# Kernel tuning notes

Hardware: AMD Instinct MI355X
Metric: run time of the kernel (lower is better)

The kernel has to match this reference:

```python
import jax, jax.numpy as jnp
import numpy as np

B, S, D, O, E, R = 4, 2048, 4096, 4096, 8, 16
SCALING = 32.0 / 16.0      # lora_alpha / lora_rank
MAX_THRESHOLD = 0.125      # 1 / num_experts


def setup_inputs() -> dict:
    key = jax.random.key(0)
    ks = jax.random.split(key, 8)
    return {
        "x": jax.random.normal(ks[0], (B, S, D), jnp.float32),
        "W_base": jax.random.normal(ks[1], (O, D), jnp.float32) * (1.0 / np.sqrt(D)),
        "b_base": jax.random.normal(ks[2], (O,), jnp.float32) * 0.02,
        "W_gate": jax.random.normal(ks[3], (E, D), jnp.float32) * (1.0 / np.sqrt(D)),
        "W_thr": jax.random.normal(ks[4], (D,), jnp.float32) * (1.0 / np.sqrt(D)),
        "b_thr": jax.random.normal(ks[5], (1,), jnp.float32) * 0.02,
        "A_w": jax.random.normal(ks[6], (E, R, D), jnp.float32) * (1.0 / np.sqrt(D)),
        "B_w": jax.random.normal(ks[7], (E, O, R), jnp.float32) * (1.0 / np.sqrt(R)),
    }


def reference(x, W_base, b_base, W_gate, W_thr, b_thr, A_w, B_w):
    # base linear: [B,S,O]
    base = jnp.einsum("bsd,od->bso", x, W_base) + b_base

    xf = x.reshape(-1, D)                                   # [N,D]
    gate = jax.nn.softmax(xf @ W_gate.T, axis=-1)           # [N,E]
    thr = jax.nn.sigmoid(xf @ W_thr + b_thr[0]) * MAX_THRESHOLD  # [N]
    adapted = gate - thr[:, None]                           # [N,E]
    selected = (adapted >= 0).astype(x.dtype)               # [N,E]
    w = adapted * selected
    wsum = jnp.sum(w, axis=-1, keepdims=True)
    wsum = jnp.where(wsum == 0, jnp.ones_like(wsum), wsum)
    w = w / wsum                                            # [N,E]

    # LoRA experts, dense equivalent of gather/compute/scatter
    h = jnp.einsum("nd,erd->ner", xf, A_w)                  # [N,E,R]
    moe = jnp.einsum("ner,ne,eor->no", h, w, B_w) * SCALING  # [N,O]

    return base + moe.reshape(base.shape)
```

## Files before the change

kernel.cpp:

```cpp
#include <hip/hip_runtime.h>
#include <hip/hip_bf16.h>

typedef float  f32x4  __attribute__((ext_vector_type(4)));
typedef __bf16 bf16x8 __attribute__((ext_vector_type(8)));
typedef __bf16 bf16x4 __attribute__((ext_vector_type(4)));

#define N_TOK 8192
#define D_DIM 4096
#define O_DIM 4096
#define ER    128
#define KCAT  4224
#define BAUX_ROWS 160

__device__ __forceinline__ void gl_lds16(const void* g, void* l) {
  __builtin_amdgcn_global_load_lds(
      (const __attribute__((address_space(1))) void*)g,
      (__attribute__((address_space(3))) void*)l, 16, 0, 0);
}

__global__ __launch_bounds__(256) void convert_kernel(
    const float* __restrict__ x,  const float* __restrict__ Wb,
    const float* __restrict__ Bw, const float* __restrict__ Aw,
    const float* __restrict__ Wg, const float* __restrict__ Wthr,
    __bf16* __restrict__ xcat, __bf16* __restrict__ Wcat,
    __bf16* __restrict__ Baux)
{
  const int id = blockIdx.x * 256 + threadIdx.x;
  const float* src;
  __bf16* dst;
  if (id < 4194304) {
    int row = id >> 9, ch = id & 511;
    src = x + ((size_t)row << 12) + ch * 8;
    dst = xcat + (size_t)row * KCAT + ch * 8;
  } else if (id < 6291456) {
    int i2 = id - 4194304;
    int row = i2 >> 9, ch = i2 & 511;
    src = Wb + ((size_t)row << 12) + ch * 8;
    dst = Wcat + (size_t)row * KCAT + ch * 8;
  } else if (id < 6356992) {
    int i2 = id - 6291456;
    int o = i2 >> 4, ch = i2 & 15;
    int e = ch >> 1, r0 = (ch & 1) * 8;
    src = Bw + (((size_t)e << 12) + o) * 16 + r0;
    dst = Wcat + (size_t)o * KCAT + D_DIM + ch * 8;
  } else {
    int i2 = id - 6356992;
    int row = i2 >> 9, ch = i2 & 511;
    dst = Baux + ((size_t)row << 12) + ch * 8;
    if (row < 128)       src = Aw + ((size_t)row << 12) + ch * 8;
    else if (row < 136)  src = Wg + ((size_t)(row - 128) << 12) + ch * 8;
    else if (row == 136) src = Wthr + ch * 8;
    else {
      bf16x8 z = {};
      *(bf16x8*)dst = z;
      return;
    }
  }
  f32x4 a = *(const f32x4*)src;
  f32x4 b = *(const f32x4*)(src + 4);
  bf16x8 v = { (__bf16)a[0], (__bf16)a[1], (__bf16)a[2], (__bf16)a[3],
               (__bf16)b[0], (__bf16)b[1], (__bf16)b[2], (__bf16)b[3] };
  *(bf16x8*)dst = v;
}

__global__ __launch_bounds__(256) void gemm_aux(
    const __bf16* __restrict__ A,
    const __bf16* __restrict__ Bm,
    float* __restrict__ pbuf, int kchunk)
{
  __shared__ __bf16 As[128 * 64];
  __shared__ __bf16 Bs[BAUX_ROWS * 64];
  const int tid  = threadIdx.x;
  const int lane = tid & 63;
  const int wave = tid >> 6;
  const int wm = wave >> 1, wn = wave & 1;
  const int quad = lane >> 4, m16 = lane & 15;
  const int bm = blockIdx.x;
  const int kc = blockIdx.y;

  f32x4 acc[4][5] = {};

  for (int k0 = kc * kchunk; k0 < (kc + 1) * kchunk; k0 += 64) {
#pragma unroll
    for (int i = 0; i < 4; ++i) {
      int c = i * 256 + tid;
      int row = c >> 3;
      int gk = (c & 7) ^ (row & 7);
      gl_lds16(A + (size_t)(bm * 128 + row) * KCAT + k0 + gk * 8, As + c * 8);
    }
#pragma unroll
    for (int i = 0; i < 5; ++i) {
      int c = i * 256 + tid;
      int row = c >> 3;
      int gk = (c & 7) ^ (row & 7);
      gl_lds16(Bm + ((size_t)row << 12) + k0 + gk * 8, Bs + c * 8);
    }
    __syncthreads();
#pragma unroll
    for (int kk = 0; kk < 64; kk += 32) {
      bf16x8 af[4], bfr[5];
#pragma unroll
      for (int i = 0; i < 4; ++i) {
        int rr = wm * 64 + i * 16 + m16;
        int ck = (kk >> 3) + quad;
        af[i] = *(const bf16x8*)(As + rr * 64 + ((ck ^ (rr & 7)) * 8));
      }
#pragma unroll
      for (int j = 0; j < 5; ++j) {
        int rr = wn * 80 + j * 16 + m16;
        int ck = (kk >> 3) + quad;
        bfr[j] = *(const bf16x8*)(Bs + rr * 64 + ((ck ^ (rr & 7)) * 8));
      }
#pragma unroll
      for (int i = 0; i < 4; ++i)
#pragma unroll
        for (int j = 0; j < 5; ++j)
          acc[i][j] = __builtin_amdgcn_mfma_f32_16x16x32_bf16(af[i], bfr[j], acc[i][j], 0, 0, 0);
    }
    __syncthreads();
  }

#pragma unroll
  for (int j = 0; j < 5; ++j) {
    int col = wn * 80 + j * 16 + m16;
#pragma unroll
    for (int i = 0; i < 4; ++i) {
      int row0 = bm * 128 + wm * 64 + i * 16 + quad * 4;
#pragma unroll
      for (int r = 0; r < 4; ++r)
        pbuf[((size_t)kc * N_TOK + row0 + r) * BAUX_ROWS + col] = acc[i][j][r];
    }
  }
}

__global__ __launch_bounds__(256) void combine_kernel(
    const float* __restrict__ pbuf,
    const float* __restrict__ bthr,
    __bf16* __restrict__ xcat, int KC)
{
  const int tid = threadIdx.x;
  const int tok = tid >> 4, l16 = tid & 15;
  const int row = blockIdx.x * 16 + tok;

  __shared__ float logits[16][9];
  __shared__ float wts[16][8];

  float h[8];
  float lg = 0.f;
#pragma unroll
  for (int i = 0; i < 8; ++i) {
    int c = i * 16 + l16;
    float s = 0.f;
    for (int kc = 0; kc < KC; ++kc)
      s += pbuf[((size_t)kc * N_TOK + row) * BAUX_ROWS + c];
    h[i] = s;
  }
  {
    int c = 128 + l16;
    for (int kc = 0; kc < KC; ++kc)
      lg += pbuf[((size_t)kc * N_TOK + row) * BAUX_ROWS + c];
    if (l16 < 9) logits[tok][l16] = lg;
  }
  __syncthreads();
  if (l16 == 0) {
    float g[9];
#pragma unroll
    for (int e = 0; e < 9; ++e) g[e] = logits[tok][e];
    float m = g[0];
#pragma unroll
    for (int e = 1; e < 8; ++e) m = fmaxf(m, g[e]);
    float p[8], s = 0.f;
#pragma unroll
    for (int e = 0; e < 8; ++e) { p[e] = expf(g[e] - m); s += p[e]; }
    float thr = 0.125f / (1.f + expf(-(g[8] + bthr[0])));
    float ws = 0.f;
#pragma unroll
    for (int e = 0; e < 8; ++e) {
      float a = p[e] / s - thr;
      a = (a >= 0.f) ? a : 0.f;
      p[e] = a; ws += a;
    }
    if (ws == 0.f) ws = 1.f;
    float inv = 2.0f / ws;
#pragma unroll
    for (int e = 0; e < 8; ++e) wts[tok][e] = p[e] * inv;
  }
  __syncthreads();
#pragma unroll
  for (int i = 0; i < 8; ++i) {
    int c = i * 16 + l16;
    xcat[(size_t)row * KCAT + D_DIM + c] = (__bf16)(h[i] * wts[tok][c >> 4]);
  }
}

__global__ __launch_bounds__(256) void gemm_main(
    const __bf16* __restrict__ A,
    const __bf16* __restrict__ Bm,
    const float* __restrict__ bias,
    float* __restrict__ out)
{
  __shared__ __bf16 As[128 * 64];
  __shared__ __bf16 Bs[128 * 64];
  const int tid  = threadIdx.x;
  const int lane = tid & 63;
  const int wave = tid >> 6;
  const int wm = wave >> 1, wn = wave & 1;
  const int quad = lane >> 4, m16 = lane & 15;

  const int bid = blockIdx.x;
  const int group = bid >> 10;
  const int r_ = bid & 1023;
  const int bn = (group << 4) | (r_ & 15);
  const int bm = r_ >> 4;

  f32x4 acc[4][4] = {};

  for (int k0 = 0; k0 < KCAT; k0 += 64) {
#pragma unroll
    for (int i = 0; i < 4; ++i) {
      int c = i * 256 + tid;
      int row = c >> 3;
      int gk = (c & 7) ^ (row & 7);
      gl_lds16(A  + (size_t)(bm * 128 + row) * KCAT + k0 + gk * 8, As + c * 8);
      gl_lds16(Bm + (size_t)(bn * 128 + row) * KCAT + k0 + gk * 8, Bs + c * 8);
    }
    __syncthreads();
#pragma unroll
    for (int kk = 0; kk < 64; kk += 32) {
      bf16x8 af[4], bfr[4];
#pragma unroll
      for (int i = 0; i < 4; ++i) {
        int rr = wm * 64 + i * 16 + m16;
        int ck = (kk >> 3) + quad;
        af[i] = *(const bf16x8*)(As + rr * 64 + ((ck ^ (rr & 7)) * 8));
      }
#pragma unroll
      for (int j = 0; j < 4; ++j) {
        int rr = wn * 64 + j * 16 + m16;
        int ck = (kk >> 3) + quad;
        bfr[j] = *(const bf16x8*)(Bs + rr * 64 + ((ck ^ (rr & 7)) * 8));
      }
#pragma unroll
      for (int i = 0; i < 4; ++i)
#pragma unroll
        for (int j = 0; j < 4; ++j)
          acc[i][j] = __builtin_amdgcn_mfma_f32_16x16x32_bf16(af[i], bfr[j], acc[i][j], 0, 0, 0);
    }
    __syncthreads();
  }

#pragma unroll
  for (int j = 0; j < 4; ++j) {
    int col = bn * 128 + wn * 64 + j * 16 + m16;
    float bv = bias[col];
#pragma unroll
    for (int i = 0; i < 4; ++i) {
      int row0 = bm * 128 + wm * 64 + i * 16 + quad * 4;
#pragma unroll
      for (int r = 0; r < 4; ++r) {
        out[(size_t)(row0 + r) * O_DIM + col] = acc[i][j][r] + bv;
      }
    }
  }
}

extern "C" void kernel_launch(void* const* d_in, const int* in_sizes, int n_in,
                              void* d_out, int out_size, void* d_ws, size_t ws_size,
                              hipStream_t stream) {
  const float* x    = (const float*)d_in[0];
  const float* Wb   = (const float*)d_in[1];
  const float* bb   = (const float*)d_in[2];
  const float* Wg   = (const float*)d_in[3];
  const float* Wthr = (const float*)d_in[4];
  const float* bthr = (const float*)d_in[5];
  const float* Aw   = (const float*)d_in[6];
  const float* Bw   = (const float*)d_in[7];
  float* out = (float*)d_out;

  char* ws = (char*)d_ws;
  __bf16* xcat = (__bf16*)ws;
  __bf16* Wcat = (__bf16*)(ws + 69206016);
  __bf16* Baux = (__bf16*)(ws + 69206016 + 34603008);
  float*  pbuf = (float*)(ws + 105119744);

  int KC = 1;
  if (ws_size >= 105119744 + 4ull * 5242880) KC = 4;
  else if (ws_size >= 105119744 + 2ull * 5242880) KC = 2;

  convert_kernel<<<25152, 256, 0, stream>>>(x, Wb, Bw, Aw, Wg, Wthr, xcat, Wcat, Baux);
  dim3 agrid(64, KC);
  gemm_aux<<<agrid, 256, 0, stream>>>(xcat, Baux, pbuf, D_DIM / KC);
  combine_kernel<<<512, 256, 0, stream>>>(pbuf, bthr, xcat, KC);
  gemm_main<<<2048, 256, 0, stream>>>(xcat, Wcat, bb, out);
}
```

Before: 651.3 us.

## Rewrite main GEMM with 256x256 tiles and a 4-stage LDS pipeline

The main bf16 GEMM now uses 512-thread workgroups computing 256x256 output tiles, where it used 128x128. K-step loads go through a 4-slot ring of LDS buffers, prefetched two steps ahead with global_load_lds and waited on via explicit vmcnt and a single barrier per step. It also adds a rotating LDS swizzle, s_setprio around the MFMA block, and an XCD-aware block remap. The goal is more operand reuse per LDS load and overlap of memory traffic with MFMA work, at the cost of higher register pressure (128 accumulators per lane) and far fewer workgroups (512).

```diff
diff --git a/kernel.cpp b/kernel.cpp
--- a/kernel.cpp
+++ b/kernel.cpp
@@ -11,6 +11,7 @@
 #define ER    128
 #define KCAT  4224
 #define BAUX_ROWS 160
+#define NT_MAIN 132
 
 __device__ __forceinline__ void gl_lds16(const void* g, void* l) {
   __builtin_amdgcn_global_load_lds(
@@ -193,69 +194,106 @@
   }
 }
 
-__global__ __launch_bounds__(256) void gemm_main(
+__global__ __launch_bounds__(512, 2) void gemm_main(
     const __bf16* __restrict__ A,
     const __bf16* __restrict__ Bm,
     const float* __restrict__ bias,
     float* __restrict__ out)
 {
-  __shared__ __bf16 As[128 * 64];
-  __shared__ __bf16 Bs[128 * 64];
+  __shared__ __bf16 As[4][256 * 32];
+  __shared__ __bf16 Bs[4][256 * 32];
+
   const int tid  = threadIdx.x;
   const int lane = tid & 63;
   const int wave = tid >> 6;
-  const int wm = wave >> 1, wn = wave & 1;
+  const int wm = wave >> 2;
+  const int wn = wave & 3;
   const int quad = lane >> 4, m16 = lane & 15;
 
-  const int bid = blockIdx.x;
-  const int group = bid >> 10;
-  const int r_ = bid & 1023;
-  const int bn = (group << 4) | (r_ & 15);
-  const int bm = r_ >> 4;
-
-  f32x4 acc[4][4] = {};
-
-  for (int k0 = 0; k0 < KCAT; k0 += 64) {
-#pragma unroll
-    for (int i = 0; i < 4; ++i) {
-      int c = i * 256 + tid;
-      int row = c >> 3;
-      int gk = (c & 7) ^ (row & 7);
-      gl_lds16(A  + (size_t)(bm * 128 + row) * KCAT + k0 + gk * 8, As + c * 8);
-      gl_lds16(Bm + (size_t)(bn * 128 + row) * KCAT + k0 + gk * 8, Bs + c * 8);
-    }
-    __syncthreads();
-#pragma unroll
-    for (int kk = 0; kk < 64; kk += 32) {
-      bf16x8 af[4], bfr[4];
-#pragma unroll
-      for (int i = 0; i < 4; ++i) {
-        int rr = wm * 64 + i * 16 + m16;
-        int ck = (kk >> 3) + quad;
-        af[i] = *(const bf16x8*)(As + rr * 64 + ((ck ^ (rr & 7)) * 8));
-      }
-#pragma unroll
-      for (int j = 0; j < 4; ++j) {
-        int rr = wn * 64 + j * 16 + m16;
-        int ck = (kk >> 3) + quad;
-        bfr[j] = *(const bf16x8*)(Bs + rr * 64 + ((ck ^ (rr & 7)) * 8));
-      }
-#pragma unroll
-      for (int i = 0; i < 4; ++i)
-#pragma unroll
-        for (int j = 0; j < 4; ++j)
-          acc[i][j] = __builtin_amdgcn_mfma_f32_16x16x32_bf16(af[i], bfr[j], acc[i][j], 0, 0, 0);
-    }
-    __syncthreads();
-  }
-
+  const int bid  = blockIdx.x;
+  const int wgid = (bid & 7) * 64 + (bid >> 3);
+  const int bm = wgid & 31;
+  const int bn = wgid >> 5;
+
+  const int c0 = tid, c1 = 512 + tid;
+  const int r0 = c0 >> 2, p0 = c0 & 3, k0 = (p0 - (r0 >> 1)) & 3;
+  const int r1 = c1 >> 2, p1 = c1 & 3, k1 = (p1 - (r1 >> 1)) & 3;
+  const __bf16* a0 = A  + (size_t)(bm * 256 + r0) * KCAT + k0 * 8;
+  const __bf16* a1 = A  + (size_t)(bm * 256 + r1) * KCAT + k1 * 8;
+  const __bf16* b0 = Bm + (size_t)(bn * 256 + r0) * KCAT + k0 * 8;
+  const __bf16* b1 = Bm + (size_t)(bn * 256 + r1) * KCAT + k1 * 8;
+  const int dc0 = c0 * 8, dc1 = c1 * 8;
+
+  int aoff[8], boff[4];
+#pragma unroll
+  for (int i = 0; i < 8; ++i) {
+    int r = wm * 128 + i * 16 + m16;
+    aoff[i] = r * 32 + (((quad + (r >> 1)) & 3) * 8);
+  }
 #pragma unroll
   for (int j = 0; j < 4; ++j) {
-    int col = bn * 128 + wn * 64 + j * 16 + m16;
+    int r = wn * 64 + j * 16 + m16;
+    boff[j] = r * 32 + (((quad + (r >> 1)) & 3) * 8);
+  }
+
+  f32x4 acc[8][4] = {};
+
+  gl_lds16(a0, &As[0][dc0]);
+  gl_lds16(a1, &As[0][dc1]);
+  gl_lds16(b0, &Bs[0][dc0]);
+  gl_lds16(b1, &Bs[0][dc1]);
+  gl_lds16(a0 + 32, &As[1][dc0]);
+  gl_lds16(a1 + 32, &As[1][dc1]);
+  gl_lds16(b0 + 32, &Bs[1][dc0]);
+  gl_lds16(b1 + 32, &Bs[1][dc1]);
+  asm volatile("s_waitcnt vmcnt(4)" ::: "memory");
+  __builtin_amdgcn_sched_barrier(0);
+  __builtin_amdgcn_s_barrier();
+  __builtin_amdgcn_sched_barrier(0);
+
+  for (int t = 0; t < NT_MAIN; ++t) {
+    if (t + 2 < NT_MAIN) {
+      const int s2 = (t + 2) & 3;
+      const int ko = (t + 2) * 32;
+      gl_lds16(a0 + ko, &As[s2][dc0]);
+      gl_lds16(a1 + ko, &As[s2][dc1]);
+      gl_lds16(b0 + ko, &Bs[s2][dc0]);
+      gl_lds16(b1 + ko, &Bs[s2][dc1]);
+    }
+
+    const __bf16* as = As[t & 3];
+    const __bf16* bs = Bs[t & 3];
+    bf16x8 af[8], bfr[4];
+#pragma unroll
+    for (int i = 0; i < 8; ++i) af[i] = *(const bf16x8*)(as + aoff[i]);
+#pragma unroll
+    for (int j = 0; j < 4; ++j) bfr[j] = *(const bf16x8*)(bs + boff[j]);
+
+    __builtin_amdgcn_s_setprio(1);
+#pragma unroll
+    for (int i = 0; i < 8; ++i)
+#pragma unroll
+      for (int j = 0; j < 4; ++j)
+        acc[i][j] = __builtin_amdgcn_mfma_f32_16x16x32_bf16(af[i], bfr[j], acc[i][j], 0, 0, 0);
+    __builtin_amdgcn_s_setprio(0);
+
+    if (t + 2 < NT_MAIN) {
+      asm volatile("s_waitcnt vmcnt(4)" ::: "memory");
+    } else {
+      asm volatile("s_waitcnt vmcnt(0)" ::: "memory");
+    }
+    __builtin_amdgcn_sched_barrier(0);
+    __builtin_amdgcn_s_barrier();
+    __builtin_amdgcn_sched_barrier(0);
+  }
+
+#pragma unroll
+  for (int j = 0; j < 4; ++j) {
+    int col = bn * 256 + wn * 64 + j * 16 + m16;
     float bv = bias[col];
 #pragma unroll
-    for (int i = 0; i < 4; ++i) {
-      int row0 = bm * 128 + wm * 64 + i * 16 + quad * 4;
+    for (int i = 0; i < 8; ++i) {
+      int row0 = bm * 256 + wm * 128 + i * 16 + quad * 4;
 #pragma unroll
       for (int r = 0; r < 4; ++r) {
         out[(size_t)(row0 + r) * O_DIM + col] = acc[i][j][r] + bv;
@@ -291,5 +329,5 @@
   dim3 agrid(64, KC);
   gemm_aux<<<agrid, 256, 0, stream>>>(xcat, Baux, pbuf, D_DIM / KC);
   combine_kernel<<<512, 256, 0, stream>>>(pbuf, bthr, xcat, KC);
-  gemm_main<<<2048, 256, 0, stream>>>(xcat, Wcat, bb, out);
-}
+  gemm_main<<<512, 512, 0, stream>>>(xcat, Wcat, bb, out);
+}
```

Result: slower. 670.0 us (+2.9%).
